# Kernel optimization log

Hardware: AMD Instinct MI355X
Metric: run time of the kernel (lower is better)

## Reference

```python
import jax, jax.numpy as jnp
import numpy as np

B, N, E, H, L = 1, 1024, 32, 1024, 8  # batch, num concepts, dim_edge, dim_hidden, stack_len


def setup_inputs() -> dict:
    key = jax.random.key(0)
    k = jax.random.split(key, 12)
    vision_feat = jax.random.normal(k[0], (B, 36, H), jnp.float32)   # unused by forward
    feat = jax.random.normal(k[1], (B, N - 1, N, E), jnp.float32)
    feat_edge = jax.random.normal(k[2], (B, 1, N, E), jnp.float32)
    c_i = jax.random.normal(k[3], (B, H), jnp.float32)
    relation_mask = jnp.ones((B, N), jnp.float32)                    # only its size is read
    att_stack = jax.random.uniform(k[4], (B, N, N, L), dtype=jnp.float32)
    sp = jax.random.uniform(k[5], (B, L), dtype=jnp.float32)
    stack_ptr = sp / jnp.sum(sp, axis=-1, keepdims=True)             # soft stack pointer
    mem_in = jax.random.normal(k[6], (B, H), jnp.float32)
    mono_mask = (jax.random.uniform(k[7], (B, N, N, 1)) > 0.5).astype(jnp.float32)
    cross_mask = jax.random.uniform(k[8], (E,), dtype=jnp.float32)
    w_c = jax.random.normal(k[9], (E, H), jnp.float32) / np.sqrt(H).astype(np.float32)
    b_c = jax.random.normal(k[10], (E,), jnp.float32) * 0.01
    return {"vision_feat": vision_feat, "feat": feat, "feat_edge": feat_edge,
            "c_i": c_i, "relation_mask": relation_mask, "att_stack": att_stack,
            "stack_ptr": stack_ptr, "mem_in": mem_in, "mono_mask": mono_mask,
            "cross_mask": cross_mask, "w_c": w_c, "b_c": b_c}


def reference(vision_feat, feat, feat_edge, c_i, relation_mask, att_stack,
              stack_ptr, mem_in, mono_mask, cross_mask, w_c, b_c):
    b = feat_edge.shape[0]
    # query = map_c(c_i).view(B,1,1,-1).expand_as(feat_edge)
    query = (c_i @ w_c.T + b_c).reshape(b, 1, 1, -1)
    query = jnp.broadcast_to(query, feat_edge.shape)                 # (B,1,N,E)
    I = jnp.concatenate([query, feat], axis=1)                       # (B,N,N,E)
    # Fusion: -(x-y)^2 + relu(x+y), feat_edge broadcasts over dim1
    elt_prod = -(I - feat_edge) ** 2 + jax.nn.relu(I + feat_edge)    # (B,N,N,E)
    weit_matrix = mono_mask * elt_prod                               # (B,N,N,E)
    # soft stack read + permute(0,2,1): att_in[b,y,x] = sum_l att_stack[b,x,y,l]*ptr[b,l]
    att_in = jnp.einsum('bxyl,bl->byx', att_stack, stack_ptr)        # (B,N,N)
    # (att_in @ weit_matrix) @ cross_mask, then permute(0,2,1).
    # Contract the edge dim first (mathematically identical by linearity).
    wv = jnp.einsum('bmye,e->bmy', weit_matrix, cross_mask)          # (B,N,N)
    att_out = jnp.einsum('bxy,bmy->bxm', att_in, wv)                 # (B,N,N)
    # max-normalize with detached norm clamped to >= 1
    norm = jax.lax.stop_gradient(jnp.max(att_out, axis=1, keepdims=True))
    norm = jnp.where(norm <= 1, jnp.ones_like(norm), norm)
    att_out = att_out / norm
    # soft stack write
    ptr = stack_ptr[:, None, None, :]                                # (B,1,1,L)
    att_stack_new = att_out[..., None] * ptr + att_stack * (1 - ptr) # (B,N,N,L)
    return att_stack_new, stack_ptr, jnp.zeros_like(mem_in)
```

## Files before the change

kernel.cpp:

```cpp
#include <hip/hip_runtime.h>
#include <math.h>

#define N 1024
#define E 32
#define L 8

__global__ __launch_bounds__(256) void k_query_tail(
    const float* __restrict__ c_i, const float* __restrict__ w_c,
    const float* __restrict__ b_c, const float* __restrict__ ptr,
    float* __restrict__ query, float* __restrict__ out_tail) {
  int b = blockIdx.x;
  if (b < 32) {
    int e = b;
    float s = 0.f;
    for (int h = threadIdx.x; h < N; h += 256)
      s += c_i[h] * w_c[e * N + h];
    #pragma unroll
    for (int off = 32; off > 0; off >>= 1)
      s += __shfl_down(s, off, 64);
    __shared__ float red[4];
    if ((threadIdx.x & 63) == 0) red[threadIdx.x >> 6] = s;
    __syncthreads();
    if (threadIdx.x == 0)
      query[e] = red[0] + red[1] + red[2] + red[3] + b_c[e];
  } else {
    if (threadIdx.x < 8) out_tail[threadIdx.x] = ptr[threadIdx.x];
    for (int i = threadIdx.x; i < N; i += 256) out_tail[8 + i] = 0.f;
  }
}

__global__ __launch_bounds__(256) void k_wv(
    const float* __restrict__ feat, const float* __restrict__ fe,
    const float* __restrict__ mono, const float* __restrict__ cm,
    const float* __restrict__ query, float* __restrict__ wv) {
  int gid = blockIdx.x * 256 + threadIdx.x;
  int m = gid >> 10;
  int y = gid & (N - 1);
  const float4* src = (m == 0)
      ? (const float4*)query
      : (const float4*)(feat + ((size_t)(m - 1) * N + y) * E);
  const float4* fev = (const float4*)(fe + (size_t)y * E);
  const float4* cmv = (const float4*)cm;
  float s = 0.f;
  #pragma unroll
  for (int j = 0; j < E / 4; ++j) {
    float4 a = src[j];
    float4 f = fev[j];
    float4 c = cmv[j];
    float dx = a.x - f.x, dy = a.y - f.y, dz = a.z - f.z, dw = a.w - f.w;
    s += c.x * (fmaxf(a.x + f.x, 0.f) - dx * dx);
    s += c.y * (fmaxf(a.y + f.y, 0.f) - dy * dy);
    s += c.z * (fmaxf(a.z + f.z, 0.f) - dz * dz);
    s += c.w * (fmaxf(a.w + f.w, 0.f) - dw * dw);
  }
  wv[gid] = mono[gid] * s;
}

__global__ __launch_bounds__(256) void k_P(
    const float* __restrict__ att_stack, const float* __restrict__ ptr,
    float* __restrict__ P) {
  int gid = blockIdx.x * 256 + threadIdx.x;
  const float4* a = (const float4*)(att_stack + (size_t)gid * L);
  float4 a0 = a[0], a1 = a[1];
  float s = a0.x * ptr[0] + a0.y * ptr[1] + a0.z * ptr[2] + a0.w * ptr[3]
          + a1.x * ptr[4] + a1.y * ptr[5] + a1.z * ptr[6] + a1.w * ptr[7];
  P[gid] = s;
}

#define BK 16
#define KCHUNK 256
__global__ __launch_bounds__(256) void k_mm(
    const float* __restrict__ P, const float* __restrict__ wv,
    float* __restrict__ Cp) {
  __shared__ float As[BK][64];
  __shared__ float Bs[BK][68];
  int tid = threadIdx.x;
  int x0 = blockIdx.x * 64;
  int m0 = blockIdx.y * 64;
  int kb = blockIdx.z * KCHUNK;
  int tx = tid & 15;
  int ty = tid >> 4;
  int la_k = tid >> 4;
  int la_c = (tid & 15) * 4;
  int lb_n = tid >> 2;
  int lb_k = (tid & 3) * 4;
  float acc[4][4] = {};
  for (int k0 = kb; k0 < kb + KCHUNK; k0 += BK) {
    float4 av = *(const float4*)&P[(size_t)(k0 + la_k) * N + x0 + la_c];
    float4 bv = *(const float4*)&wv[(size_t)(m0 + lb_n) * N + k0 + lb_k];
    __syncthreads();
    *(float4*)&As[la_k][la_c] = av;
    Bs[lb_k + 0][lb_n] = bv.x;
    Bs[lb_k + 1][lb_n] = bv.y;
    Bs[lb_k + 2][lb_n] = bv.z;
    Bs[lb_k + 3][lb_n] = bv.w;
    __syncthreads();
    #pragma unroll
    for (int k = 0; k < BK; ++k) {
      float4 a = *(const float4*)&As[k][ty * 4];
      float4 b = *(const float4*)&Bs[k][tx * 4];
      float ar[4] = {a.x, a.y, a.z, a.w};
      float br[4] = {b.x, b.y, b.z, b.w};
      #pragma unroll
      for (int r = 0; r < 4; ++r)
        #pragma unroll
        for (int c = 0; c < 4; ++c)
          acc[r][c] = fmaf(ar[r], br[c], acc[r][c]);
    }
  }
  float* Cc = Cp + (size_t)blockIdx.z * N * N;
  #pragma unroll
  for (int r = 0; r < 4; ++r) {
    float4 o = {acc[r][0], acc[r][1], acc[r][2], acc[r][3]};
    *(float4*)&Cc[(size_t)(x0 + ty * 4 + r) * N + m0 + tx * 4] = o;
  }
}

__global__ __launch_bounds__(1024) void k_rednorm(
    const float* __restrict__ Cp, float* __restrict__ C,
    float* __restrict__ normp) {
  int m = threadIdx.x;
  int xg = blockIdx.x;
  float mx = -INFINITY;
  #pragma unroll
  for (int j = 0; j < 8; ++j) {
    size_t idx = (size_t)(xg * 8 + j) * N + m;
    float s = Cp[idx] + Cp[idx + (size_t)N * N] + Cp[idx + (size_t)2 * N * N]
            + Cp[idx + (size_t)3 * N * N];
    C[idx] = s;
    mx = fmaxf(mx, s);
  }
  normp[(size_t)xg * N + m] = mx;
}

__global__ __launch_bounds__(256) void k_norm2(
    const float* __restrict__ normp, float* __restrict__ norm) {
  int m = blockIdx.x * 256 + threadIdx.x;
  float mx = -INFINITY;
  #pragma unroll 8
  for (int xg = 0; xg < 128; ++xg)
    mx = fmaxf(mx, normp[(size_t)xg * N + m]);
  norm[m] = (mx <= 1.f) ? 1.f : mx;
}

__global__ __launch_bounds__(256) void k_blend(
    const float* __restrict__ C, const float* __restrict__ norm,
    const float* __restrict__ att_stack, const float* __restrict__ ptr,
    float* __restrict__ out) {
  int gid = blockIdx.x * 256 + threadIdx.x;
  int m = gid & (N - 1);
  float a = C[gid] / norm[m];
  const float4* s = (const float4*)(att_stack + (size_t)gid * L);
  float4 s0 = s[0], s1 = s[1];
  float p0 = ptr[0], p1 = ptr[1], p2 = ptr[2], p3 = ptr[3];
  float p4 = ptr[4], p5 = ptr[5], p6 = ptr[6], p7 = ptr[7];
  float4 o0, o1;
  o0.x = a * p0 + s0.x * (1.f - p0);
  o0.y = a * p1 + s0.y * (1.f - p1);
  o0.z = a * p2 + s0.z * (1.f - p2);
  o0.w = a * p3 + s0.w * (1.f - p3);
  o1.x = a * p4 + s1.x * (1.f - p4);
  o1.y = a * p5 + s1.y * (1.f - p5);
  o1.z = a * p6 + s1.z * (1.f - p6);
  o1.w = a * p7 + s1.w * (1.f - p7);
  float4* o = (float4*)(out + (size_t)gid * L);
  o[0] = o0;
  o[1] = o1;
}

extern "C" void kernel_launch(void* const* d_in, const int* in_sizes, int n_in,
                              void* d_out, int out_size, void* d_ws, size_t ws_size,
                              hipStream_t stream) {
  const float* feat      = (const float*)d_in[1];
  const float* feat_edge = (const float*)d_in[2];
  const float* c_i       = (const float*)d_in[3];
  const float* att_stack = (const float*)d_in[5];
  const float* stack_ptr = (const float*)d_in[6];
  const float* mono_mask = (const float*)d_in[8];
  const float* cross_mask= (const float*)d_in[9];
  const float* w_c       = (const float*)d_in[10];
  const float* b_c       = (const float*)d_in[11];

  float* out = (float*)d_out;
  float* ws  = (float*)d_ws;

  float* query = ws;
  float* wv    = ws + 64;
  float* P     = wv + (size_t)N * N;
  float* C     = P + (size_t)N * N;
  float* norm  = C + (size_t)N * N;
  float* normp = norm + 1024;
  float* Cp    = normp + (size_t)128 * N;

  float* out_tail = out + (size_t)N * N * L;

  k_query_tail<<<33, 256, 0, stream>>>(c_i, w_c, b_c, stack_ptr, query, out_tail);
  k_wv<<<(N * N) / 256, 256, 0, stream>>>(feat, feat_edge, mono_mask, cross_mask,
                                          query, wv);
  k_P<<<(N * N) / 256, 256, 0, stream>>>(att_stack, stack_ptr, P);
  dim3 mmgrid(16, 16, 4);
  k_mm<<<mmgrid, 256, 0, stream>>>(P, wv, Cp);
  k_rednorm<<<128, 1024, 0, stream>>>(Cp, C, normp);
  k_norm2<<<4, 256, 0, stream>>>(normp, norm);
  k_blend<<<(N * N) / 256, 256, 0, stream>>>(C, norm, att_stack, stack_ptr, out);
}
```

Before: 337.8 us.

## Use split-bf16 MFMA for matmul and fuse query, wv and P prep into one kernel

```diff
diff --git a/kernel.cpp b/kernel.cpp
--- a/kernel.cpp
+++ b/kernel.cpp
@@ -4,116 +4,169 @@
 #define N 1024
 #define E 32
 #define L 8
-
-__global__ __launch_bounds__(256) void k_query_tail(
-    const float* __restrict__ c_i, const float* __restrict__ w_c,
-    const float* __restrict__ b_c, const float* __restrict__ ptr,
-    float* __restrict__ query, float* __restrict__ out_tail) {
-  int b = blockIdx.x;
-  if (b < 32) {
-    int e = b;
-    float s = 0.f;
-    for (int h = threadIdx.x; h < N; h += 256)
-      s += c_i[h] * w_c[e * N + h];
-    #pragma unroll
-    for (int off = 32; off > 0; off >>= 1)
-      s += __shfl_down(s, off, 64);
-    __shared__ float red[4];
-    if ((threadIdx.x & 63) == 0) red[threadIdx.x >> 6] = s;
-    __syncthreads();
-    if (threadIdx.x == 0)
-      query[e] = red[0] + red[1] + red[2] + red[3] + b_c[e];
-  } else {
-    if (threadIdx.x < 8) out_tail[threadIdx.x] = ptr[threadIdx.x];
-    for (int i = threadIdx.x; i < N; i += 256) out_tail[8 + i] = 0.f;
-  }
-}
-
-__global__ __launch_bounds__(256) void k_wv(
+#define NN ((size_t)N * N)
+
+using short8 = __attribute__((ext_vector_type(8))) short;
+using f32x4v = __attribute__((ext_vector_type(4))) float;
+
+__device__ inline ushort2 split_bf16(float v) {
+  unsigned ui = __float_as_uint(v);
+  ushort h = (ushort)(ui >> 16);
+  float hv = __uint_as_float((unsigned)h << 16);
+  float r = v - hv;
+  ushort l = (ushort)(__float_as_uint(r) >> 16);
+  return make_ushort2(h, l);
+}
+
+__device__ inline void gload16(const void* g, void* l) {
+  __builtin_amdgcn_global_load_lds(
+      (const __attribute__((address_space(1))) unsigned int*)g,
+      (__attribute__((address_space(3))) unsigned int*)l, 16, 0, 0);
+}
+
+__global__ __launch_bounds__(256) void k_prep(
     const float* __restrict__ feat, const float* __restrict__ fe,
     const float* __restrict__ mono, const float* __restrict__ cm,
-    const float* __restrict__ query, float* __restrict__ wv) {
-  int gid = blockIdx.x * 256 + threadIdx.x;
-  int m = gid >> 10;
-  int y = gid & (N - 1);
-  const float4* src = (m == 0)
-      ? (const float4*)query
-      : (const float4*)(feat + ((size_t)(m - 1) * N + y) * E);
-  const float4* fev = (const float4*)(fe + (size_t)y * E);
-  const float4* cmv = (const float4*)cm;
-  float s = 0.f;
+    const float* __restrict__ c_i, const float* __restrict__ w_c,
+    const float* __restrict__ b_c, const float* __restrict__ att_stack,
+    const float* __restrict__ ptr,
+    ushort* __restrict__ wv_h, ushort* __restrict__ wv_l,
+    ushort* __restrict__ Pt_h, ushort* __restrict__ Pt_l,
+    float* __restrict__ out_tail) {
+  __shared__ __align__(16) float qsm[32];
+  __shared__ ushort Ts[2][64][66];
+  int b = blockIdx.x;
+  int tid = threadIdx.x;
+  if (b < 4096) {
+    int gid = b * 256 + tid;
+    int m = gid >> 10;
+    int y = gid & (N - 1);
+    if (b < 4) {
+      int e = tid >> 3, r = tid & 7;
+      float s = 0.f;
+      for (int h = r; h < N; h += 8) s += c_i[h] * w_c[e * N + h];
+      #pragma unroll
+      for (int off = 4; off > 0; off >>= 1) s += __shfl_down(s, off, 8);
+      if (r == 0) qsm[e] = s + b_c[e];
+      __syncthreads();
+    }
+    const float* src = (m == 0)
+        ? (const float*)qsm
+        : (feat + ((size_t)(m - 1) * N + y) * E);
+    const float4* sv  = (const float4*)src;
+    const float4* fev = (const float4*)(fe + (size_t)y * E);
+    const float4* cmv = (const float4*)cm;
+    float s = 0.f;
+    #pragma unroll
+    for (int j = 0; j < E / 4; ++j) {
+      float4 a = sv[j];
+      float4 f = fev[j];
+      float4 c = cmv[j];
+      float dx = a.x - f.x, dy = a.y - f.y, dz = a.z - f.z, dw = a.w - f.w;
+      s += c.x * (fmaxf(a.x + f.x, 0.f) - dx * dx);
+      s += c.y * (fmaxf(a.y + f.y, 0.f) - dy * dy);
+      s += c.z * (fmaxf(a.z + f.z, 0.f) - dz * dz);
+      s += c.w * (fmaxf(a.w + f.w, 0.f) - dw * dw);
+    }
+    float v = mono[gid] * s;
+    ushort2 hl = split_bf16(v);
+    wv_h[gid] = hl.x;
+    wv_l[gid] = hl.y;
+  } else if (b < 4096 + 256) {
+    int pb = b - 4096;
+    int j0 = (pb >> 4) * 64;
+    int i0 = (pb & 15) * 64;
+    float p0 = ptr[0], p1 = ptr[1], p2 = ptr[2], p3 = ptr[3];
+    float p4 = ptr[4], p5 = ptr[5], p6 = ptr[6], p7 = ptr[7];
+    int w = tid >> 6, lane = tid & 63;
+    #pragma unroll 4
+    for (int r = 0; r < 16; ++r) {
+      int jl = r * 4 + w;
+      int il = lane;
+      const float4* a =
+          (const float4*)(att_stack + ((size_t)(j0 + jl) * N + i0 + il) * L);
+      float4 a0 = a[0], a1 = a[1];
+      float s = a0.x * p0 + a0.y * p1 + a0.z * p2 + a0.w * p3
+              + a1.x * p4 + a1.y * p5 + a1.z * p6 + a1.w * p7;
+      ushort2 hl = split_bf16(s);
+      Ts[0][il][jl] = hl.x;
+      Ts[1][il][jl] = hl.y;
+    }
+    __syncthreads();
+    int il = tid >> 2, c = tid & 3;
+    size_t o = (size_t)(i0 + il) * N + j0 + c * 16;
+    {
+      const uint* sp = (const uint*)&Ts[0][il][c * 16];
+      uint4 d0 = {sp[0], sp[1], sp[2], sp[3]};
+      uint4 d1 = {sp[4], sp[5], sp[6], sp[7]};
+      *(uint4*)&Pt_h[o] = d0;
+      *(uint4*)&Pt_h[o + 8] = d1;
+    }
+    {
+      const uint* sp = (const uint*)&Ts[1][il][c * 16];
+      uint4 d0 = {sp[0], sp[1], sp[2], sp[3]};
+      uint4 d1 = {sp[4], sp[5], sp[6], sp[7]};
+      *(uint4*)&Pt_l[o] = d0;
+      *(uint4*)&Pt_l[o + 8] = d1;
+    }
+  } else {
+    if (tid < 8) out_tail[tid] = ptr[tid];
+    for (int i = tid; i < N; i += 256) out_tail[8 + i] = 0.f;
+  }
+}
+
+__global__ __launch_bounds__(256) void k_mm(
+    const ushort* __restrict__ Pt_h, const ushort* __restrict__ Pt_l,
+    const ushort* __restrict__ wv_h, const ushort* __restrict__ wv_l,
+    float* __restrict__ Cp) {
+  __shared__ ushort As[2][64][32];
+  __shared__ ushort Bs[2][64][32];
+  int tid = threadIdx.x;
+  int lane = tid & 63, w = tid >> 6;
+  int x0 = blockIdx.x * 64, m0 = blockIdx.y * 64;
+  int kb = blockIdx.z * 256;
+  int srow = w * 16 + (lane >> 2);
+  int scol = (lane & 3) * 8;
+  const ushort* gAh = Pt_h + (size_t)(x0 + srow) * N + kb + scol;
+  const ushort* gAl = Pt_l + (size_t)(x0 + srow) * N + kb + scol;
+  const ushort* gBh = wv_h + (size_t)(m0 + srow) * N + kb + scol;
+  const ushort* gBl = wv_l + (size_t)(m0 + srow) * N + kb + scol;
+  ushort* lAh = &As[0][w * 16][0];
+  ushort* lAl = &As[1][w * 16][0];
+  ushort* lBh = &Bs[0][w * 16][0];
+  ushort* lBl = &Bs[1][w * 16][0];
+  int fr = w * 16 + (lane & 15);
+  int fk = (lane >> 4) * 8;
+  int fn = lane & 15;
+  f32x4v acc[4];
   #pragma unroll
-  for (int j = 0; j < E / 4; ++j) {
-    float4 a = src[j];
-    float4 f = fev[j];
-    float4 c = cmv[j];
-    float dx = a.x - f.x, dy = a.y - f.y, dz = a.z - f.z, dw = a.w - f.w;
-    s += c.x * (fmaxf(a.x + f.x, 0.f) - dx * dx);
-    s += c.y * (fmaxf(a.y + f.y, 0.f) - dy * dy);
-    s += c.z * (fmaxf(a.z + f.z, 0.f) - dz * dz);
-    s += c.w * (fmaxf(a.w + f.w, 0.f) - dw * dw);
+  for (int t = 0; t < 4; ++t) acc[t] = (f32x4v){0.f, 0.f, 0.f, 0.f};
+  for (int kt = 0; kt < 8; ++kt) {
+    __syncthreads();
+    gload16(gAh + kt * 32, lAh);
+    gload16(gAl + kt * 32, lAl);
+    gload16(gBh + kt * 32, lBh);
+    gload16(gBl + kt * 32, lBl);
+    __syncthreads();
+    short8 Ah = *(const short8*)&As[0][fr][fk];
+    short8 Al = *(const short8*)&As[1][fr][fk];
+    #pragma unroll
+    for (int t = 0; t < 4; ++t) {
+      short8 Bh = *(const short8*)&Bs[0][t * 16 + fn][fk];
+      short8 Bl = *(const short8*)&Bs[1][t * 16 + fn][fk];
+      acc[t] = __builtin_amdgcn_mfma_f32_16x16x32_bf16(Ah, Bh, acc[t], 0, 0, 0);
+      acc[t] = __builtin_amdgcn_mfma_f32_16x16x32_bf16(Ah, Bl, acc[t], 0, 0, 0);
+      acc[t] = __builtin_amdgcn_mfma_f32_16x16x32_bf16(Al, Bh, acc[t], 0, 0, 0);
+    }
   }
-  wv[gid] = mono[gid] * s;
-}
-
-__global__ __launch_bounds__(256) void k_P(
-    const float* __restrict__ att_stack, const float* __restrict__ ptr,
-    float* __restrict__ P) {
-  int gid = blockIdx.x * 256 + threadIdx.x;
-  const float4* a = (const float4*)(att_stack + (size_t)gid * L);
-  float4 a0 = a[0], a1 = a[1];
-  float s = a0.x * ptr[0] + a0.y * ptr[1] + a0.z * ptr[2] + a0.w * ptr[3]
-          + a1.x * ptr[4] + a1.y * ptr[5] + a1.z * ptr[6] + a1.w * ptr[7];
-  P[gid] = s;
-}
-
-#define BK 16
-#define KCHUNK 256
-__global__ __launch_bounds__(256) void k_mm(
-    const float* __restrict__ P, const float* __restrict__ wv,
-    float* __restrict__ Cp) {
-  __shared__ float As[BK][64];
-  __shared__ float Bs[BK][68];
-  int tid = threadIdx.x;
-  int x0 = blockIdx.x * 64;
-  int m0 = blockIdx.y * 64;
-  int kb = blockIdx.z * KCHUNK;
-  int tx = tid & 15;
-  int ty = tid >> 4;
-  int la_k = tid >> 4;
-  int la_c = (tid & 15) * 4;
-  int lb_n = tid >> 2;
-  int lb_k = (tid & 3) * 4;
-  float acc[4][4] = {};
-  for (int k0 = kb; k0 < kb + KCHUNK; k0 += BK) {
-    float4 av = *(const float4*)&P[(size_t)(k0 + la_k) * N + x0 + la_c];
-    float4 bv = *(const float4*)&wv[(size_t)(m0 + lb_n) * N + k0 + lb_k];
-    __syncthreads();
-    *(float4*)&As[la_k][la_c] = av;
-    Bs[lb_k + 0][lb_n] = bv.x;
-    Bs[lb_k + 1][lb_n] = bv.y;
-    Bs[lb_k + 2][lb_n] = bv.z;
-    Bs[lb_k + 3][lb_n] = bv.w;
-    __syncthreads();
+  float* Cc = Cp + (size_t)blockIdx.z * NN;
+  int orow = x0 + w * 16 + (lane >> 4) * 4;
+  int ocol = m0 + fn;
+  #pragma unroll
+  for (int t = 0; t < 4; ++t)
     #pragma unroll
-    for (int k = 0; k < BK; ++k) {
-      float4 a = *(const float4*)&As[k][ty * 4];
-      float4 b = *(const float4*)&Bs[k][tx * 4];
-      float ar[4] = {a.x, a.y, a.z, a.w};
-      float br[4] = {b.x, b.y, b.z, b.w};
-      #pragma unroll
-      for (int r = 0; r < 4; ++r)
-        #pragma unroll
-        for (int c = 0; c < 4; ++c)
-          acc[r][c] = fmaf(ar[r], br[c], acc[r][c]);
-    }
-  }
-  float* Cc = Cp + (size_t)blockIdx.z * N * N;
-  #pragma unroll
-  for (int r = 0; r < 4; ++r) {
-    float4 o = {acc[r][0], acc[r][1], acc[r][2], acc[r][3]};
-    *(float4*)&Cc[(size_t)(x0 + ty * 4 + r) * N + m0 + tx * 4] = o;
-  }
+    for (int r = 0; r < 4; ++r)
+      Cc[(size_t)(orow + r) * N + ocol + t * 16] = acc[t][r];
 }
 
 __global__ __launch_bounds__(1024) void k_rednorm(
@@ -123,10 +176,9 @@
   int xg = blockIdx.x;
   float mx = -INFINITY;
   #pragma unroll
-  for (int j = 0; j < 8; ++j) {
-    size_t idx = (size_t)(xg * 8 + j) * N + m;
-    float s = Cp[idx] + Cp[idx + (size_t)N * N] + Cp[idx + (size_t)2 * N * N]
-            + Cp[idx + (size_t)3 * N * N];
+  for (int j = 0; j < 4; ++j) {
+    size_t idx = (size_t)(xg * 4 + j) * N + m;
+    float s = Cp[idx] + Cp[idx + NN] + Cp[idx + 2 * NN] + Cp[idx + 3 * NN];
     C[idx] = s;
     mx = fmaxf(mx, s);
   }
@@ -138,7 +190,7 @@
   int m = blockIdx.x * 256 + threadIdx.x;
   float mx = -INFINITY;
   #pragma unroll 8
-  for (int xg = 0; xg < 128; ++xg)
+  for (int xg = 0; xg < 256; ++xg)
     mx = fmaxf(mx, normp[(size_t)xg * N + m]);
   norm[m] = (mx <= 1.f) ? 1.f : mx;
 }
@@ -182,25 +234,24 @@
   const float* b_c       = (const float*)d_in[11];
 
   float* out = (float*)d_out;
-  float* ws  = (float*)d_ws;
-
-  float* query = ws;
-  float* wv    = ws + 64;
-  float* P     = wv + (size_t)N * N;
-  float* C     = P + (size_t)N * N;
-  float* norm  = C + (size_t)N * N;
-  float* normp = norm + 1024;
-  float* Cp    = normp + (size_t)128 * N;
-
-  float* out_tail = out + (size_t)N * N * L;
-
-  k_query_tail<<<33, 256, 0, stream>>>(c_i, w_c, b_c, stack_ptr, query, out_tail);
-  k_wv<<<(N * N) / 256, 256, 0, stream>>>(feat, feat_edge, mono_mask, cross_mask,
-                                          query, wv);
-  k_P<<<(N * N) / 256, 256, 0, stream>>>(att_stack, stack_ptr, P);
+
+  ushort* wv_h = (ushort*)d_ws;
+  ushort* wv_l = wv_h + NN;
+  ushort* Pt_h = wv_l + NN;
+  ushort* Pt_l = Pt_h + NN;
+  float*  Cp   = (float*)(Pt_l + NN);
+  float*  C    = Cp + 4 * NN;
+  float*  normp= C + NN;
+  float*  norm = normp + (size_t)256 * N;
+
+  float* out_tail = out + NN * L;
+
+  k_prep<<<4353, 256, 0, stream>>>(feat, feat_edge, mono_mask, cross_mask,
+                                   c_i, w_c, b_c, att_stack, stack_ptr,
+                                   wv_h, wv_l, Pt_h, Pt_l, out_tail);
   dim3 mmgrid(16, 16, 4);
-  k_mm<<<mmgrid, 256, 0, stream>>>(P, wv, Cp);
-  k_rednorm<<<128, 1024, 0, stream>>>(Cp, C, normp);
+  k_mm<<<mmgrid, 256, 0, stream>>>(Pt_h, Pt_l, wv_h, wv_l, Cp);
+  k_rednorm<<<256, 1024, 0, stream>>>(Cp, C, normp);
   k_norm2<<<4, 256, 0, stream>>>(normp, norm);
-  k_blend<<<(N * N) / 256, 256, 0, stream>>>(C, norm, att_stack, stack_ptr, out);
-}
+  k_blend<<<4096, 256, 0, stream>>>(C, norm, att_stack, stack_ptr, out);
+}
```

Measured after the change: 332.9 us. Within noise of the previous version (-1.4%).
